# Optimization experiments

Measured on AMD Instinct MI355X. Metric: run time of the kernel, lower is better.

Reference implementation:

```python
import jax, jax.numpy as jnp
import numpy as np


def setup_inputs() -> dict:
    key = jax.random.key(0)
    B, N = 4, 32768
    xyz = jax.random.normal(key, (B, N, 3), dtype=jnp.float32)
    return {"xyz": xyz, "K": 16, "nqueries": 2048}


def reference(xyz, K, nqueries):
    # xyz: (b, n, 3). Deterministic strided pick of nqueries query points
    # (stand-in for the KD-tree's distance-pick sampling), then brute-force KNN.
    b, n, _ = xyz.shape
    stride = n // nqueries
    q_idx = jnp.arange(nqueries) * stride          # (nq,)
    pts = xyz[:, q_idx, :]                          # (b, nq, 3) sampled query points
    # pairwise squared distances (b, nq, n)
    d = jnp.sum((pts[:, :, None, :] - xyz[:, None, :, :]) ** 2, axis=-1)
    _, idx = jax.lax.top_k(-d, K)                   # (b, nq, K) nearest-neighbor indices
    idx = idx.astype(jnp.int64)[..., None]          # (b, nq, K, 1) matches expand_dims(..., 3)
    return idx, pts
```

## Files before the change

kernel.cpp:

```cpp
#include <hip/hip_runtime.h>
#include <stdint.h>

#define NPTS  32768
#define NQ    2048
#define KNN   16
#define NB    4
#define BLOCK 256
#define WPB   4
#define PPL   8
#define ITERS (NPTS / (64 * PPL))

__device__ __forceinline__ int dpp_shr1_i(int x) {
    return __builtin_amdgcn_update_dpp(x, x, 0x111, 0xf, 0xf, false);
}
__device__ __forceinline__ float dpp_shr1_f(float x) {
    return __int_as_float(dpp_shr1_i(__float_as_int(x)));
}
__device__ __forceinline__ float readlane_f(float x, int l) {
    return __int_as_float(__builtin_amdgcn_readlane(__float_as_int(x), l));
}

template <int T>
__device__ __forceinline__ void insert_all(float d, int p, int lane,
                                           float& ld, int& li, float& tau, float& tg)
{
    unsigned long long rem = __ballot(d <= tau);
    while (rem) {
        const int srcl = __ffsll(rem) - 1;
        const float wd = readlane_f(d, srcl);
        const int   wi = __builtin_amdgcn_readlane(p, srcl);
        const bool less = (ld < wd) || (ld == wd && li < wi);
        const unsigned long long lm = __ballot(less);
        const int pos = __popc((unsigned)((lm >> (16 * T)) & 0xffffull));
        const float pld = dpp_shr1_f(ld);
        const int   pli = dpp_shr1_i(li);
        if ((lane >> 4) == T) {
            const int gl = lane & 15;
            if (gl == pos)      { ld = wd;  li = wi;  }
            else if (gl > pos)  { ld = pld; li = pli; }
        }
        tau = readlane_f(ld, 16 * T + 15);
        tg  = tau * 1.00001f;
        rem &= rem - 1;
        if (rem) rem &= __ballot(d <= tau);
    }
}

__device__ __forceinline__ void load6(float4 dst[6], const float4* p) {
    #pragma unroll
    for (int t = 0; t < 6; ++t) dst[t] = p[t];
}

__device__ __forceinline__ void step(const float4 c[6], int pb, int lane,
                                     float qx0, float qy0, float qz0,
                                     float qx1, float qy1, float qz1,
                                     float& ld, int& li,
                                     float& tau0, float& tau1,
                                     float& tg0, float& tg1)
{
    float px[PPL], py[PPL], pz[PPL];
    px[0] = c[0].x; py[0] = c[0].y; pz[0] = c[0].z;
    px[1] = c[0].w; py[1] = c[1].x; pz[1] = c[1].y;
    px[2] = c[1].z; py[2] = c[1].w; pz[2] = c[2].x;
    px[3] = c[2].y; py[3] = c[2].z; pz[3] = c[2].w;
    px[4] = c[3].x; py[4] = c[3].y; pz[4] = c[3].z;
    px[5] = c[3].w; py[5] = c[4].x; pz[5] = c[4].y;
    px[6] = c[4].z; py[6] = c[4].w; pz[6] = c[5].x;
    px[7] = c[5].y; py[7] = c[5].z; pz[7] = c[5].w;

    unsigned long long m0[PPL], m1[PPL], any = 0;
    #pragma unroll
    for (int j = 0; j < PPL; ++j) {
        const float ax = px[j] - qx0, ay = py[j] - qy0, az = pz[j] - qz0;
        const float g0 = __fmaf_rn(az, az, __fmaf_rn(ay, ay, __fmul_rn(ax, ax)));
        m0[j] = __ballot(g0 <= tg0);
        const float bx = px[j] - qx1, by = py[j] - qy1, bz = pz[j] - qz1;
        const float g1 = __fmaf_rn(bz, bz, __fmaf_rn(by, by, __fmul_rn(bx, bx)));
        m1[j] = __ballot(g1 <= tg1);
        any |= m0[j] | m1[j];
    }
    if (any) {
        #pragma unroll
        for (int j = 0; j < PPL; ++j) {
            if (m0[j]) {
                const float dx = __fadd_rn(px[j], -qx0);
                const float dy = __fadd_rn(py[j], -qy0);
                const float dz = __fadd_rn(pz[j], -qz0);
                const float d  = __fadd_rn(
                    __fadd_rn(__fmul_rn(dx, dx), __fmul_rn(dy, dy)),
                    __fmul_rn(dz, dz));
                insert_all<0>(d, pb + j, lane, ld, li, tau0, tg0);
            }
        }
        #pragma unroll
        for (int j = 0; j < PPL; ++j) {
            if (m1[j]) {
                const float dx = __fadd_rn(px[j], -qx1);
                const float dy = __fadd_rn(py[j], -qy1);
                const float dz = __fadd_rn(pz[j], -qz1);
                const float d  = __fadd_rn(
                    __fadd_rn(__fmul_rn(dx, dx), __fmul_rn(dy, dy)),
                    __fmul_rn(dz, dz));
                insert_all<1>(d, pb + j, lane, ld, li, tau1, tg1);
            }
        }
    }
}

__global__ __launch_bounds__(BLOCK, 4) void knn_kernel(const float* __restrict__ xyz,
                                                       float* __restrict__ out_idx,
                                                       float* __restrict__ out_pts)
{
    const int tid  = threadIdx.x;
    const int lane = tid & 63;
    const int wv   = tid >> 6;
    const int w    = blockIdx.x * WPB + wv;
    const int b    = w >> 10;
    const int pr   = w & 1023;
    const size_t base = (size_t)b * NPTS * 3;

    const int qp0 = pr << 5;
    const float qx0 = xyz[base + 3 * qp0 + 0];
    const float qy0 = xyz[base + 3 * qp0 + 1];
    const float qz0 = xyz[base + 3 * qp0 + 2];
    const float qx1 = xyz[base + 3 * qp0 + 48];
    const float qy1 = xyz[base + 3 * qp0 + 49];
    const float qz1 = xyz[base + 3 * qp0 + 50];

    const int g0 = b * NQ + (pr << 1);
    if (lane == 0) {
        out_pts[3 * g0 + 0] = qx0;
        out_pts[3 * g0 + 1] = qy0;
        out_pts[3 * g0 + 2] = qz0;
        out_pts[3 * g0 + 3] = qx1;
        out_pts[3 * g0 + 4] = qy1;
        out_pts[3 * g0 + 5] = qz1;
    }

    float ld = __builtin_inff();  int li = 0x7fffffff;
    float tau0 = __builtin_inff(), tau1 = __builtin_inff();
    float tg0  = __builtin_inff(), tg1  = __builtin_inff();

    const float4* lp = (const float4*)(xyz + base) + 6 * lane;

    float4 A[6], Bf[6];
    load6(A, lp);
    for (int k = 0; k < ITERS; k += 2) {
        load6(Bf, lp + 384);
        step(A, (k << 9) + PPL * lane, lane,
             qx0, qy0, qz0, qx1, qy1, qz1, ld, li, tau0, tau1, tg0, tg1);
        if (k + 2 < ITERS)
            load6(A, lp + 768);
        step(Bf, ((k + 1) << 9) + PPL * lane, lane,
             qx0, qy0, qz0, qx1, qy1, qz1, ld, li, tau0, tau1, tg0, tg1);
        lp += 768;
    }

    if (lane < 2 * KNN) {
        out_idx[(size_t)g0 * KNN + lane] = (float)li;
    }
}

extern "C" void kernel_launch(void* const* d_in, const int* in_sizes, int n_in,
                              void* d_out, int out_size, void* d_ws, size_t ws_size,
                              hipStream_t stream) {
    const float* xyz = (const float*)d_in[0];
    float* out = (float*)d_out;
    float* out_idx = out;
    float* out_pts = out + (size_t)NB * NQ * KNN;

    const int blocks = (NB * NQ / 2) / WPB;
    knn_kernel<<<blocks, BLOCK, 0, stream>>>(xyz, out_idx, out_pts);
}
```

Measured before the change: 196.1 us.

## Split point scan across two waves per query pair and merge top-K in LDS

Each query pair is now handled by a 128-thread block whose two waves each scan half of the point cloud and keep their own sorted top-16 lists. The two partial lists are merged through shared memory with a rank-counting merge, where each element counts the smaller entries in the other list to find its output slot. This doubles the wave count and halves the serial scan length per wave, which should improve latency hiding and load balance. In exchange each wave's pruning threshold tightens more slowly, so more insertions happen, and a block barrier plus merge step is added.

```diff
diff --git a/kernel.cpp b/kernel.cpp
--- a/kernel.cpp
+++ b/kernel.cpp
@@ -5,10 +5,11 @@
 #define NQ    2048
 #define KNN   16
 #define NB    4
-#define BLOCK 256
-#define WPB   4
+#define BLOCK 128
+#define WPB   2
 #define PPL   8
-#define ITERS (NPTS / (64 * PPL))
+#define HALF  (NPTS / 2)
+#define ITERS_H (HALF / (64 * PPL))
 
 __device__ __forceinline__ int dpp_shr1_i(int x) {
     return __builtin_amdgcn_update_dpp(x, x, 0x111, 0xf, 0xf, false);
@@ -107,16 +108,16 @@
     }
 }
 
-__global__ __launch_bounds__(BLOCK, 4) void knn_kernel(const float* __restrict__ xyz,
+__global__ __launch_bounds__(BLOCK, 8) void knn_kernel(const float* __restrict__ xyz,
                                                        float* __restrict__ out_idx,
                                                        float* __restrict__ out_pts)
 {
     const int tid  = threadIdx.x;
     const int lane = tid & 63;
-    const int wv   = tid >> 6;
-    const int w    = blockIdx.x * WPB + wv;
-    const int b    = w >> 10;
-    const int pr   = w & 1023;
+    const int half = tid >> 6;
+    const int pair = blockIdx.x;
+    const int b    = pair >> 10;
+    const int pr   = pair & 1023;
     const size_t base = (size_t)b * NPTS * 3;
 
     const int qp0 = pr << 5;
@@ -128,7 +129,7 @@
     const float qz1 = xyz[base + 3 * qp0 + 50];
 
     const int g0 = b * NQ + (pr << 1);
-    if (lane == 0) {
+    if (half == 0 && lane == 0) {
         out_pts[3 * g0 + 0] = qx0;
         out_pts[3 * g0 + 1] = qy0;
         out_pts[3 * g0 + 2] = qz0;
@@ -141,23 +142,43 @@
     float tau0 = __builtin_inff(), tau1 = __builtin_inff();
     float tg0  = __builtin_inff(), tg1  = __builtin_inff();
 
-    const float4* lp = (const float4*)(xyz + base) + 6 * lane;
+    const int pbase = half * HALF;
+    const float4* lp = (const float4*)(xyz + base) + half * (HALF * 3 / 4) + 6 * lane;
 
     float4 A[6], Bf[6];
     load6(A, lp);
-    for (int k = 0; k < ITERS; k += 2) {
+    for (int k = 0; k < ITERS_H; k += 2) {
         load6(Bf, lp + 384);
-        step(A, (k << 9) + PPL * lane, lane,
+        step(A, pbase + (k << 9) + PPL * lane, lane,
              qx0, qy0, qz0, qx1, qy1, qz1, ld, li, tau0, tau1, tg0, tg1);
-        if (k + 2 < ITERS)
+        if (k + 2 < ITERS_H)
             load6(A, lp + 768);
-        step(Bf, ((k + 1) << 9) + PPL * lane, lane,
+        step(Bf, pbase + ((k + 1) << 9) + PPL * lane, lane,
              qx0, qy0, qz0, qx1, qy1, qz1, ld, li, tau0, tau1, tg0, tg1);
         lp += 768;
     }
 
-    if (lane < 2 * KNN) {
-        out_idx[(size_t)g0 * KNN + lane] = (float)li;
+    __shared__ float sd[WPB * 32];
+    __shared__ int   si[WPB * 32];
+    if (lane < 32) {
+        sd[(half << 5) + lane] = ld;
+        si[(half << 5) + lane] = li;
+    }
+    __syncthreads();
+    if (lane < 32) {
+        const int T  = lane >> 4;
+        const int r  = lane & 15;
+        const int pb2 = ((half ^ 1) << 5) + (T << 4);
+        int cnt = 0;
+        #pragma unroll
+        for (int t = 0; t < 16; ++t) {
+            const float od = sd[pb2 + t];
+            const int   oi = si[pb2 + t];
+            cnt += (od < ld || (od == ld && oi < li)) ? 1 : 0;
+        }
+        const int pos = r + cnt;
+        if (pos < KNN)
+            out_idx[((size_t)(g0 + T)) * KNN + pos] = (float)li;
     }
 }
 
@@ -169,6 +190,6 @@
     float* out_idx = out;
     float* out_pts = out + (size_t)NB * NQ * KNN;
 
-    const int blocks = (NB * NQ / 2) / WPB;
+    const int blocks = NB * NQ / 2;
     knn_kernel<<<blocks, BLOCK, 0, stream>>>(xyz, out_idx, out_pts);
 }
```

Result: slower. 642.8 us (+227.8%).
